# Kernel tuning notes

Hardware: AMD Instinct MI355X
Metric: run time of the kernel (lower is better)

Reference implementation:

```python
import jax, jax.numpy as jnp
import numpy as np

ALPHA, GAMMA = 0.25, 2.0            # focal loss params (cfg defaults)
W_CLASS, W_BBOX, W_GIOU = 2.0, 5.0, 2.0
N_CANDIDATE_K = 5                   # top-k ious used to derive dynamic k
CENTER_RADIUS = 2.5
B, Q, G, C = 32, 2000, 64, 80
IMG_W, IMG_H = 1333.0, 800.0


def _box_iou(a, b):
    # a: [Q,4] xyxy, b: [G,4] xyxy -> iou [Q,G], union [Q,G]
    area_a = (a[:, 2] - a[:, 0]) * (a[:, 3] - a[:, 1])
    area_b = (b[:, 2] - b[:, 0]) * (b[:, 3] - b[:, 1])
    lt = jnp.maximum(a[:, None, :2], b[None, :, :2])
    rb = jnp.minimum(a[:, None, 2:], b[None, :, 2:])
    wh = jnp.clip(rb - lt, 0.0)
    inter = wh[..., 0] * wh[..., 1]
    union = area_a[:, None] + area_b[None, :] - inter
    return inter / union, union


def _generalized_box_iou(a, b):
    iou, union = _box_iou(a, b)
    lt = jnp.minimum(a[:, None, :2], b[None, :, :2])
    rb = jnp.maximum(a[:, None, 2:], b[None, :, 2:])
    wh = jnp.clip(rb - lt, 0.0)
    area_c = wh[..., 0] * wh[..., 1]
    return iou - (area_c - union) / area_c


def _get_in_boxes_info(boxes, gt):
    # boxes, gt: absolute xyxy. Anchor centers inside gt box / inside center region.
    cx = (boxes[:, 0] + boxes[:, 2]) * 0.5
    cy = (boxes[:, 1] + boxes[:, 3]) * 0.5
    is_in_boxes = ((cx[:, None] > gt[None, :, 0]) & (cx[:, None] < gt[None, :, 2]) &
                   (cy[:, None] > gt[None, :, 1]) & (cy[:, None] < gt[None, :, 3]))
    gt_cx = (gt[:, 0] + gt[:, 2]) * 0.5
    gt_cy = (gt[:, 1] + gt[:, 3]) * 0.5
    gt_w = gt[:, 2] - gt[:, 0]
    gt_h = gt[:, 3] - gt[:, 1]
    is_in_centers = ((cx[:, None] > (gt_cx - CENTER_RADIUS * gt_w)[None, :]) &
                     (cx[:, None] < (gt_cx + CENTER_RADIUS * gt_w)[None, :]) &
                     (cy[:, None] > (gt_cy - CENTER_RADIUS * gt_h)[None, :]) &
                     (cy[:, None] < (gt_cy + CENTER_RADIUS * gt_h)[None, :]))
    fg_mask = is_in_boxes.any(1) | is_in_centers.any(1)
    return fg_mask, is_in_boxes & is_in_centers


def _dedup(cost, matching):
    # queries matched to >1 gt keep only their min-cost gt
    over = matching.sum(1) > 1
    keep = jax.nn.one_hot(jnp.argmin(cost, axis=1), cost.shape[1], dtype=matching.dtype)
    return jnp.where(over[:, None], keep, matching)


def _dynamic_k_matching(cost, ious):
    Qn, Gn = cost.shape
    topk_ious = jax.lax.top_k(ious.T, N_CANDIDATE_K)[0]              # [G,k]
    dynamic_ks = jnp.maximum(topk_ious.sum(1).astype(jnp.int32), 1)  # [G]
    # rank of each query within each gt's cost column (ascending)
    ranks = jnp.argsort(jnp.argsort(cost, axis=0), axis=0)
    matching = (ranks < dynamic_ks[None, :]).astype(cost.dtype)      # [Q,G]
    matching = _dedup(cost, matching)

    # ensure every gt gets >=1 query; bounded loop replaces data-dependent while
    def body(_, carry):
        cost_c, match_c = carry
        unmatched = match_c.sum(0) == 0                              # [G]
        any_un = unmatched.any()
        matched_q = match_c.sum(1) > 0
        cost_n = cost_c + jnp.where(matched_q, 1e5, 0.0)[:, None]
        add = jax.nn.one_hot(jnp.argmin(cost_n, axis=0), Qn, dtype=match_c.dtype).T
        match_n = jnp.maximum(match_c, add * unmatched[None, :].astype(match_c.dtype))
        match_n = _dedup(cost_n, match_n)
        return (jnp.where(any_un, cost_n, cost_c), jnp.where(any_un, match_n, match_c))

    cost, matching = jax.lax.fori_loop(0, Gn, body, (cost, matching))
    masked = jnp.where(matching > 0, cost, jnp.inf)
    matched_query_id = jnp.argmin(masked, axis=0)                    # [G]
    return matching, matched_query_id


def _match_one(logits, boxes, tgt_ids, gt_boxes, size_out, size_tgt):
    fg_mask, in_bc = _get_in_boxes_info(boxes, gt_boxes)
    ious, _ = _box_iou(boxes, gt_boxes)                              # [Q,G]
    neg = (1.0 - ALPHA) * logits ** GAMMA * (-jnp.log(1.0 - logits + 1e-8))
    pos = ALPHA * (1.0 - logits) ** GAMMA * (-jnp.log(logits + 1e-8))
    cost_class = jnp.take(pos - neg, tgt_ids, axis=1)                # [Q,G]
    out_n = boxes / size_out                                         # [Q,4]
    tgt_n = gt_boxes / size_tgt                                      # [G,4]
    cost_bbox = jnp.abs(out_n[:, None, :] - tgt_n[None, :, :]).sum(-1)  # L1 cdist
    cost_giou = -_generalized_box_iou(boxes, gt_boxes)
    cost = (W_BBOX * cost_bbox + W_CLASS * cost_class + W_GIOU * cost_giou
            + 100.0 * (~in_bc).astype(cost_bbox.dtype))
    cost = cost + jnp.where(fg_mask, 0.0, 1e4)[:, None]
    return _dynamic_k_matching(cost, ious)


def _rand_boxes(key, n_shape):
    k1, k2 = jax.random.split(key)
    wh = jnp.array([IMG_W, IMG_H], jnp.float32)
    ctr = jax.random.uniform(k1, n_shape + (2,)) * wh
    size = jax.random.uniform(k2, n_shape + (2,)) * (wh * 0.3) + 8.0
    x1y1 = jnp.clip(ctr - size * 0.5, 0.0, wh)
    x2y2 = jnp.clip(ctr + size * 0.5, 0.0, wh)
    x2y2 = jnp.maximum(x2y2, x1y1 + 1.0)
    return jnp.concatenate([x1y1, x2y2], axis=-1)


def setup_inputs() -> dict:
    key = jax.random.key(0)
    k1, k2, k3, k4 = jax.random.split(key, 4)
    pred_logits = jax.random.uniform(k1, (B, Q, C), minval=1e-4, maxval=1.0 - 1e-4)
    pred_boxes = _rand_boxes(k2, (B, Q))
    gt_classes = jax.random.randint(k3, (B, G), 0, C)
    gt_boxes = _rand_boxes(k4, (B, G))
    sz = jnp.array([IMG_W, IMG_H, IMG_W, IMG_H], jnp.float32)
    return {
        'pred_logits': pred_logits,
        'pred_boxes': pred_boxes,
        'gt_classes': gt_classes,
        'gt_boxes': gt_boxes,
        'image_size_xyxy': jnp.tile(sz, (B, 1)),
        'image_size_xyxy_tgt': jnp.tile(sz, (B, G, 1)),
    }


def reference(pred_logits, pred_boxes, gt_classes, gt_boxes, image_size_xyxy, image_size_xyxy_tgt):
    # matching: [B,Q,G] 0/1 assignment matrix (row q matched to gt g);
    # matched_query_id: [B,G] best query per gt. Padded-G, fixed-shape analog of
    # the per-image variable-length (indices, matched_ids) lists.
    matching, matched_query_id = jax.vmap(_match_one)(
        pred_logits, pred_boxes, gt_classes, gt_boxes, image_size_xyxy, image_size_xyxy_tgt)
    return matching, matched_query_id
```

## Files before the change

### kernel.cpp

```cpp
#include <hip/hip_runtime.h>
#include <cmath>

#pragma clang fp contract(off)

#define BB 32
#define QQ 2000
#define GG 64
#define CCH 80
#define TOPC 16
#define QT 32

typedef unsigned long long u64;

__global__ __launch_bounds__(256) void cost_kernel(
    const float* __restrict__ logits, const float* __restrict__ boxes,
    const int* __restrict__ gtc, const float* __restrict__ gtb,
    const float* __restrict__ szout, const float* __restrict__ sztgt,
    float* __restrict__ cost, int* __restrict__ rowarg,
    float* __restrict__ out_match) {
#pragma clang fp contract(off)
  const int b = blockIdx.y;
  const int q0 = blockIdx.x * QT;
  const int t = threadIdx.x;
  const int w = t >> 6, lane = t & 63;

  __shared__ float4 s_qb[QT];
  __shared__ float4 s_qn[QT];
  __shared__ float s_tile[QT * 65];

  const int gbase = (b * GG + lane) * 4;
  const float g0 = gtb[gbase + 0], g1 = gtb[gbase + 1];
  const float g2 = gtb[gbase + 2], g3 = gtb[gbase + 3];
  const float t0 = g0 / sztgt[gbase + 0], t1 = g1 / sztgt[gbase + 1];
  const float t2 = g2 / sztgt[gbase + 2], t3 = g3 / sztgt[gbase + 3];
  const float garea = (g2 - g0) * (g3 - g1);
  const float gcx = (g0 + g2) * 0.5f, gcy = (g1 + g3) * 0.5f;
  const float gw = g2 - g0, gh = g3 - g1;
  const float cxlo = gcx - 2.5f * gw, cxhi = gcx + 2.5f * gw;
  const float cylo = gcy - 2.5f * gh, cyhi = gcy + 2.5f * gh;
  const int cls = gtc[b * GG + lane];

  if (t < QT) {
    int q = q0 + t;
    float4 bx = (q < QQ) ? reinterpret_cast<const float4*>(boxes)[b * QQ + q]
                         : make_float4(0.f, 0.f, 1.f, 1.f);
    s_qb[t] = bx;
    float4 on;
    on.x = bx.x / szout[b * 4 + 0];
    on.y = bx.y / szout[b * 4 + 1];
    on.z = bx.z / szout[b * 4 + 2];
    on.w = bx.w / szout[b * 4 + 3];
    s_qn[t] = on;
  }

  const float* lbase = logits + (size_t)b * QQ * CCH;
  float pv[8];
  #pragma unroll
  for (int i = 0; i < 8; ++i) {
    int q = q0 + w * 8 + i;
    pv[i] = (q < QQ) ? lbase[(size_t)q * CCH + cls] : 0.5f;
  }
  __syncthreads();

  #pragma unroll
  for (int i = 0; i < 8; ++i) {
    const int qi = w * 8 + i;
    float4 bx = s_qb[qi];
    float4 on = s_qn[qi];
    float x1 = bx.x, y1 = bx.y, x2 = bx.z, y2 = bx.w;
    float cx = (x1 + x2) * 0.5f, cy = (y1 + y2) * 0.5f;
    float areaa = (x2 - x1) * (y2 - y1);

    bool ib = (cx > g0) & (cx < g2) & (cy > g1) & (cy < g3);
    bool ic = (cx > cxlo) & (cx < cxhi) & (cy > cylo) & (cy < cyhi);
    bool fg = (__ballot(ib) != 0ull) || (__ballot(ic) != 0ull);
    float fgadd = fg ? 0.0f : 1e4f;

    float ltx = fmaxf(x1, g0), lty = fmaxf(y1, g1);
    float rbx = fminf(x2, g2), rby = fminf(y2, g3);
    float iw = fmaxf(rbx - ltx, 0.0f), ih = fmaxf(rby - lty, 0.0f);
    float inter = iw * ih;
    float uni = (areaa + garea) - inter;
    float iou = inter / uni;
    float ex1 = fminf(x1, g0), ey1 = fminf(y1, g1);
    float ex2 = fmaxf(x2, g2), ey2 = fmaxf(y2, g3);
    float ew = fmaxf(ex2 - ex1, 0.0f), eh = fmaxf(ey2 - ey1, 0.0f);
    float areac = ew * eh;
    float giou = iou - (areac - uni) / areac;

    float p = pv[i];
    float negc = (0.75f * (p * p)) * (-logf((1.0f - p) + 1e-8f));
    float posc = (0.25f * ((1.0f - p) * (1.0f - p))) * (-logf(p + 1e-8f));
    float ccls = posc - negc;

    float cb = ((fabsf(on.x - t0) + fabsf(on.y - t1)) + fabsf(on.z - t2)) + fabsf(on.w - t3);
    float notbc = (ib & ic) ? 0.0f : 1.0f;
    float c = ((5.0f * cb + 2.0f * ccls) + 2.0f * (-giou)) + 100.0f * notbc;
    c = c + fgadd;

    s_tile[qi * 65 + lane] = c;
  }
  __syncthreads();

  if (t < QT) {
    int q = q0 + t;
    if (q < QQ) {
      const float* row = &s_tile[t * 65];
      float bv = row[0]; int bg = 0;
      #pragma unroll
      for (int g = 1; g < GG; ++g) {
        float cv = row[g];
        if (cv < bv) { bv = cv; bg = g; }
      }
      rowarg[b * QQ + q] = bg;
    }
  }

  float* cb_out = cost + (size_t)b * GG * QQ;
  const int qi = t & 31;
  const int q = q0 + qi;
  if (q < QQ) {
    #pragma unroll
    for (int pass = 0; pass < 8; ++pass) {
      int g = (t >> 5) + pass * 8;
      cb_out[(size_t)g * QQ + q] = s_tile[qi * 65 + g];
    }
  }

  int nq = QQ - q0; if (nq > QT) nq = QT;
  if (nq > 0) {
    float4* zb = reinterpret_cast<float4*>(out_match + ((size_t)b * QQ + q0) * GG);
    int n4 = nq * GG / 4;
    float4 z = make_float4(0.f, 0.f, 0.f, 0.f);
    for (int i = t; i < n4; i += 256) zb[i] = z;
  }
}

template <int TOPN>
__device__ __forceinline__ void block_select(
    u64 (&K)[8], int tid, u64* s_tmin, u64* s_cmin, u64* s_surv,
    u64* s_sorted, u64* s_thr, int* s_ns) {
  u64 m = K[0];
  #pragma unroll
  for (int j = 1; j < 8; ++j) m = (K[j] < m) ? K[j] : m;
  s_tmin[tid] = m;
  if (tid == 0) *s_ns = 0;
  __syncthreads();

  if (tid < 64) {
    u64 c = s_tmin[tid];
    u64 c1 = s_tmin[tid + 64], c2 = s_tmin[tid + 128], c3 = s_tmin[tid + 192];
    c = (c1 < c) ? c1 : c; c = (c2 < c) ? c2 : c; c = (c3 < c) ? c3 : c;
    s_cmin[tid] = c;
    int r = 0;
    for (int j = 0; j < 64; ++j) r += (s_cmin[j] < c) ? 1 : 0;
    if (r == TOPN - 1) *s_thr = c;
  }
  __syncthreads();

  const u64 t = *s_thr;
  int n = 0;
  #pragma unroll
  for (int j = 0; j < 8; ++j) n += (K[j] <= t) ? 1 : 0;
  if (n) {
    int base = atomicAdd(s_ns, n);
    int k = 0;
    #pragma unroll
    for (int j = 0; j < 8; ++j) if (K[j] <= t) s_surv[base + (k++)] = K[j];
  }
  __syncthreads();

  const int ns = *s_ns;
  if (ns <= 64) {
    if (tid < ns && tid < 64) {
      u64 k = s_surv[tid];
      int r = 0;
      for (int j = 0; j < ns; ++j) r += (s_surv[j] < k) ? 1 : 0;
      if (r < TOPN) s_sorted[r] = k;
    }
  } else if (tid < 64) {
    for (int pass = 0; pass < TOPN; ++pass) {
      u64 bk = ~0ull;
      for (int idx = tid; idx < ns; idx += 64) {
        u64 v = s_surv[idx]; bk = (v < bk) ? v : bk;
      }
      for (int off = 32; off; off >>= 1) {
        u64 ok = __shfl_down(bk, off, 64); bk = (ok < bk) ? ok : bk;
      }
      bk = __shfl(bk, 0, 64);
      for (int idx = tid; idx < ns; idx += 64)
        if (s_surv[idx] == bk) s_surv[idx] = ~0ull;
      if (tid == 0) s_sorted[pass] = bk;
    }
  }
  __syncthreads();
}

__global__ __launch_bounds__(256) void pick_kernel(
    const float* __restrict__ boxes, const float* __restrict__ gtb,
    const float* __restrict__ cost, short* __restrict__ lists,
    int* __restrict__ dynks) {
#pragma clang fp contract(off)
  const int bc = blockIdx.x;
  const int b = bc >> 6, col = bc & 63;
  const int tid = threadIdx.x;

  __shared__ u64 s_tmin[256];
  __shared__ u64 s_cmin[64];
  __shared__ u64 s_surv[512];
  __shared__ u64 s_sorted[TOPC];
  __shared__ u64 s_thr;
  __shared__ int s_ns;

  const int gbase = (b * GG + col) * 4;
  const float gx1 = gtb[gbase + 0], gy1 = gtb[gbase + 1];
  const float gx2 = gtb[gbase + 2], gy2 = gtb[gbase + 3];
  const float ga = (gx2 - gx1) * (gy2 - gy1);

  u64 K[8];
  #pragma unroll
  for (int j = 0; j < 8; ++j) {
    int q = tid * 8 + j;
    float val = -1e30f;
    if (q < QQ) {
      float4 bx = reinterpret_cast<const float4*>(boxes)[b * QQ + q];
      float areaa = (bx.z - bx.x) * (bx.w - bx.y);
      float ltx = fmaxf(bx.x, gx1), lty = fmaxf(bx.y, gy1);
      float rbx = fminf(bx.z, gx2), rby = fminf(bx.w, gy2);
      float iw = fmaxf(rbx - ltx, 0.0f), ih = fmaxf(rby - lty, 0.0f);
      float inter = iw * ih;
      val = inter / ((areaa + ga) - inter);
    }
    unsigned u = __float_as_uint(val);
    u = (u & 0x80000000u) ? ~u : (u | 0x80000000u);
    K[j] = ~(((u64)u << 16) | (u64)(0xFFFF - q));
  }
  block_select<5>(K, tid, s_tmin, s_cmin, s_surv, s_sorted, &s_thr, &s_ns);
  if (tid == 0) {
    float s = 0.0f;
    for (int r = 0; r < 5; ++r) {
      u64 kk = ~s_sorted[r];
      unsigned u = (unsigned)(kk >> 16);
      u = (u & 0x80000000u) ? (u & 0x7FFFFFFFu) : ~u;
      s += __uint_as_float(u);
    }
    int dynk = (int)s;
    if (dynk < 1) dynk = 1;
    dynks[bc] = dynk;
  }

  const float* ccol = cost + (size_t)bc * QQ;
  {
    float cv[8];
    if (tid < 249) {
      const float4* c4 = reinterpret_cast<const float4*>(ccol) + tid * 2;
      float4 a = c4[0], d = c4[1];
      cv[0] = a.x; cv[1] = a.y; cv[2] = a.z; cv[3] = a.w;
      cv[4] = d.x; cv[5] = d.y; cv[6] = d.z; cv[7] = d.w;
    } else {
      #pragma unroll
      for (int j = 0; j < 8; ++j) {
        int q = tid * 8 + j;
        cv[j] = (q < QQ) ? ccol[q] : INFINITY;
      }
    }
    #pragma unroll
    for (int j = 0; j < 8; ++j) {
      unsigned u = __float_as_uint(cv[j]);
      u = (u & 0x80000000u) ? ~u : (u | 0x80000000u);
      K[j] = ((u64)u << 16) | (u64)(tid * 8 + j);
    }
  }
  block_select<TOPC>(K, tid, s_tmin, s_cmin, s_surv, s_sorted, &s_thr, &s_ns);
  if (tid < TOPC) lists[bc * TOPC + tid] = (short)(s_sorted[tid] & 0xFFFFull);
}

__global__ __launch_bounds__(256) void serial_kernel(
    const float* __restrict__ cost, const short* __restrict__ lists,
    const int* __restrict__ dynks, const int* __restrict__ rowarg,
    float* __restrict__ out_match, float* __restrict__ out_ids) {
#pragma clang fp contract(off)
  const int b = blockIdx.x;
  const int tid = threadIdx.x;

  __shared__ unsigned s_mlo[QQ], s_mhi[QQ];
  __shared__ int s_first[QQ];
  __shared__ int s_pushed[QQ];
  __shared__ short s_rarg[QQ];
  __shared__ short s_list[GG * TOPC];
  __shared__ int s_cnt[GG];
  __shared__ short s_chosen[GG];
  __shared__ unsigned long long s_pack[GG];
  __shared__ int s_added[GG];
  __shared__ short s_ucols[GG];
  __shared__ short s_fb[GG];
  __shared__ int s_nadd, s_nfb, s_Tv;

  for (int q = tid; q < QQ; q += 256) {
    s_mlo[q] = 0u; s_mhi[q] = 0u; s_first[q] = -1; s_pushed[q] = -1;
    s_rarg[q] = (short)rowarg[b * QQ + q];
  }
  for (int i = tid; i < GG * TOPC; i += 256) s_list[i] = lists[b * GG * TOPC + i];
  if (tid < GG) s_cnt[tid] = 0;
  __syncthreads();

  if (tid < GG) {
    int dynk = dynks[b * GG + tid];
    s_cnt[tid] = dynk;
    for (int i = 0; i < dynk; ++i) {
      int q = s_list[tid * TOPC + i];
      if (tid < 32) atomicOr(&s_mlo[q], 1u << tid);
      else          atomicOr(&s_mhi[q], 1u << (tid - 32));
      s_first[q] = 0;
    }
  }
  __syncthreads();

  for (int q = tid; q < QQ; q += 256) {
    unsigned lo = s_mlo[q], hi = s_mhi[q];
    if (__popc(lo) + __popc(hi) > 1) {
      int bg = s_rarg[q];
      unsigned tl = lo, th = hi;
      while (tl) { int g = __ffs(tl) - 1; tl &= tl - 1; if (g != bg) atomicSub(&s_cnt[g], 1); }
      while (th) { int g = __ffs(th) + 31; th &= th - 1; if (g != bg) atomicSub(&s_cnt[g], 1); }
      bool had = (bg < 32) ? ((lo >> bg) & 1u) : ((hi >> (bg - 32)) & 1u);
      if (!had) atomicAdd(&s_cnt[bg], 1);
      s_mlo[q] = (bg < 32) ? (1u << bg) : 0u;
      s_mhi[q] = (bg >= 32) ? (1u << (bg - 32)) : 0u;
    }
  }
  __syncthreads();

  const float* costb = cost + (size_t)b * GG * QQ;

  if (tid < 64) {
    const int lane = tid;
    int T = 0;
    for (int iter = 0; iter < GG; ++iter) {
      unsigned long long bal = __ballot(s_cnt[lane] > 0);
      unsigned long long um = ~bal;
      if (um == 0ull) break;
      T++;

      bool isun = (um >> lane) & 1ull;
      int nu = __popcll(um);
      int pos = __popcll(um & ((1ull << lane) - 1ull));
      if (isun) s_ucols[pos] = (short)lane;
      if (lane == 0) { s_nfb = 0; s_nadd = 0; }

      const int sg = lane >> 4, li = lane & 15;
      for (int base = 0; base < nu; base += 4) {
        int ci = base + sg;
        int col = (ci < nu) ? (int)s_ucols[ci] : -1;
        bool cand_un = false; int cq = 0;
        if (col >= 0) {
          cq = s_list[col * TOPC + li];
          cand_un = ((s_mlo[cq] | s_mhi[cq]) == 0u);
        }
        unsigned long long bb = __ballot(cand_un);
        unsigned sub = (unsigned)((bb >> (sg * 16)) & 0xFFFFull);
        if (col >= 0) {
          if (sub) {
            if (li == __ffs(sub) - 1) s_chosen[col] = (short)cq;
          } else if (li == 0) {
            int slot = atomicAdd(&s_nfb, 1);
            s_fb[slot] = (short)col;
          }
        }
      }

      int nfb = s_nfb;
      for (int fi = 0; fi < nfb; ++fi) {
        int col = s_fb[fi];
        const float* ccol = costb + (size_t)col * QQ;
        float bv = INFINITY; int bq = 0x7fffffff;
        for (int q2 = lane; q2 < QQ; q2 += 64) {
          if ((s_mlo[q2] | s_mhi[q2]) == 0u) {
            float cv = ccol[q2];
            if (cv < bv) { bv = cv; bq = q2; }
          }
        }
        for (int off = 32; off; off >>= 1) {
          float ov = __shfl_down(bv, off, 64); int oq = __shfl_down(bq, off, 64);
          if (ov < bv || (ov == bv && oq < bq)) { bv = ov; bq = oq; }
        }
        bq = __shfl(bq, 0, 64);
        if (bq == 0x7fffffff) {
          bv = INFINITY; bq = 0x7fffffff;
          for (int q2 = lane; q2 < QQ; q2 += 64) {
            float cv = ccol[q2];
            int k = (s_first[q2] >= 0) ? (iter + 1 - s_first[q2]) : 0;
            for (int tt = 0; tt < k; ++tt) cv += 1e5f;
            if (cv < bv) { bv = cv; bq = q2; }
          }
          for (int off = 32; off; off >>= 1) {
            float ov = __shfl_down(bv, off, 64); int oq = __shfl_down(bq, off, 64);
            if (ov < bv || (ov == bv && oq < bq)) { bv = ov; bq = oq; }
          }
          bq = __shfl(bq, 0, 64);
        }
        if (lane == 0) s_chosen[col] = (short)bq;
      }

      if (isun) {
        int q = s_chosen[lane];
        if (lane < 32) atomicOr(&s_mlo[q], 1u << lane);
        else           atomicOr(&s_mhi[q], 1u << (lane - 32));
        atomicAdd(&s_cnt[lane], 1);
        if (s_first[q] == -1) s_first[q] = iter + 1;
        if (atomicExch(&s_pushed[q], iter) != iter) {
          int slot = atomicAdd(&s_nadd, 1);
          s_added[slot] = q;
        }
      }

      int na = s_nadd;
      if (lane < na) {
        int q = s_added[lane];
        unsigned lo = s_mlo[q], hi = s_mhi[q];
        if (__popc(lo) + __popc(hi) > 1) {
          int bg = s_rarg[q];
          unsigned tl = lo, th = hi;
          while (tl) { int g = __ffs(tl) - 1; tl &= tl - 1; if (g != bg) atomicSub(&s_cnt[g], 1); }
          while (th) { int g = __ffs(th) + 31; th &= th - 1; if (g != bg) atomicSub(&s_cnt[g], 1); }
          bool had = (bg < 32) ? ((lo >> bg) & 1u) : ((hi >> (bg - 32)) & 1u);
          if (!had) atomicAdd(&s_cnt[bg], 1);
          s_mlo[q] = (bg < 32) ? (1u << bg) : 0u;
          s_mhi[q] = (bg >= 32) ? (1u << (bg - 32)) : 0u;
        }
      }
    }
    if (tid == 0) s_Tv = T;
  }
  __syncthreads();
  const int T = s_Tv;

  if (tid < GG) s_pack[tid] = 0xFFFFFFFFFFFFFFFFull;
  __syncthreads();
  for (int q = tid; q < QQ; q += 256) {
    unsigned lo = s_mlo[q], hi = s_mhi[q];
    if (lo | hi) {
      int g = lo ? (__ffs(lo) - 1) : (__ffs(hi) + 31);
      float cv = costb[(size_t)g * QQ + q];
      int k = T - s_first[q];
      for (int tt = 0; tt < k; ++tt) cv += 1e5f;
      unsigned ub = __float_as_uint(cv);
      ub = (ub & 0x80000000u) ? ~ub : (ub | 0x80000000u);
      unsigned long long pk = ((unsigned long long)ub << 16) | (unsigned)q;
      atomicMin(&s_pack[g], pk);
    }
  }
  __syncthreads();
  if (tid < GG) {
    unsigned long long pk = s_pack[tid];
    out_ids[b * GG + tid] =
        (pk == 0xFFFFFFFFFFFFFFFFull) ? 0.0f : (float)(pk & 0xFFFFull);
  }
  for (int q = tid; q < QQ; q += 256) {
    unsigned lo = s_mlo[q], hi = s_mhi[q];
    if (lo | hi) {
      int g = lo ? (__ffs(lo) - 1) : (__ffs(hi) + 31);
      out_match[((size_t)b * QQ + q) * GG + g] = 1.0f;
    }
  }
}

extern "C" void kernel_launch(void* const* d_in, const int* in_sizes, int n_in,
                              void* d_out, int out_size, void* d_ws, size_t ws_size,
                              hipStream_t stream) {
  const float* logits = (const float*)d_in[0];
  const float* boxes  = (const float*)d_in[1];
  const int*   gtc    = (const int*)d_in[2];
  const float* gtbx   = (const float*)d_in[3];
  const float* szout  = (const float*)d_in[4];
  const float* sztgt  = (const float*)d_in[5];
  float* out = (float*)d_out;

  const size_t matchN  = (size_t)BB * QQ * GG;
  const size_t rowargN = (size_t)BB * QQ;
  const size_t listsN  = (size_t)BB * GG * TOPC;

  char* p = (char*)d_ws;
  float* cost   = (float*)p;          p += matchN * 4;
  int*   rowarg = (int*)p;            p += rowargN * 4;
  short* lists  = (short*)p;          p += listsN * 2;
  int*   dynks  = (int*)p;

  float* out_ids = out + matchN;

  hipLaunchKernelGGL(cost_kernel, dim3((QQ + QT - 1) / QT, BB), dim3(256), 0, stream,
                     logits, boxes, gtc, gtbx, szout, sztgt, cost, rowarg, out);
  hipLaunchKernelGGL(pick_kernel, dim3(BB * GG), dim3(256), 0, stream,
                     boxes, gtbx, cost, lists, dynks);
  hipLaunchKernelGGL(serial_kernel, dim3(BB), dim3(256), 0, stream,
                     cost, lists, dynks, rowarg, out, out_ids);
}
```

Before: 127.6 us.

## Restructure serial matching loop with per-lane candidate registers and matched-byte mask

The single-wave iterative matching loop now keeps each gt column's 16 top candidates in registers and tests them against a byte-per-query 'matched' mask. This replaces the cooperative 4-columns-per-pass ballot scan and the shared compaction arrays. Fallback columns are picked directly from a ballot bitmask, and the chosen query stays in a register. Duplicate detection drops the per-query atomicExch push array and uses a linear scan over the added list. The aim is to cut shared-memory traffic and synchronisation inside the latency-bound serial loop. The trade-off is extra per-lane work in the quadratic duplicate scan and the new mask, which is never cleared when a query is deduplicated.

```diff
diff --git a/kernel.cpp b/kernel.cpp
--- a/kernel.cpp
+++ b/kernel.cpp
@@ -285,33 +285,30 @@
 
   __shared__ unsigned s_mlo[QQ], s_mhi[QQ];
   __shared__ int s_first[QQ];
-  __shared__ int s_pushed[QQ];
+  __shared__ unsigned char s_mq[QQ];
   __shared__ short s_rarg[QQ];
-  __shared__ short s_list[GG * TOPC];
   __shared__ int s_cnt[GG];
-  __shared__ short s_chosen[GG];
-  __shared__ unsigned long long s_pack[GG];
+  __shared__ u64 s_pack[GG];
   __shared__ int s_added[GG];
-  __shared__ short s_ucols[GG];
-  __shared__ short s_fb[GG];
-  __shared__ int s_nadd, s_nfb, s_Tv;
+  __shared__ int s_nadd, s_Tv;
 
   for (int q = tid; q < QQ; q += 256) {
-    s_mlo[q] = 0u; s_mhi[q] = 0u; s_first[q] = -1; s_pushed[q] = -1;
+    s_mlo[q] = 0u; s_mhi[q] = 0u; s_first[q] = -1; s_mq[q] = 0;
     s_rarg[q] = (short)rowarg[b * QQ + q];
   }
-  for (int i = tid; i < GG * TOPC; i += 256) s_list[i] = lists[b * GG * TOPC + i];
   if (tid < GG) s_cnt[tid] = 0;
   __syncthreads();
 
   if (tid < GG) {
     int dynk = dynks[b * GG + tid];
     s_cnt[tid] = dynk;
+    const short* lrow = lists + (b * GG + tid) * TOPC;
     for (int i = 0; i < dynk; ++i) {
-      int q = s_list[tid * TOPC + i];
+      int q = lrow[i];
       if (tid < 32) atomicOr(&s_mlo[q], 1u << tid);
       else          atomicOr(&s_mhi[q], 1u << (tid - 32));
       s_first[q] = 0;
+      s_mq[q] = 1;
     }
   }
   __syncthreads();
@@ -335,47 +332,43 @@
 
   if (tid < 64) {
     const int lane = tid;
+    unsigned cand[8];
+    {
+      const unsigned* lrow =
+          reinterpret_cast<const unsigned*>(lists + (b * GG + lane) * TOPC);
+      #pragma unroll
+      for (int j = 0; j < 8; ++j) cand[j] = lrow[j];
+    }
     int T = 0;
     for (int iter = 0; iter < GG; ++iter) {
       unsigned long long bal = __ballot(s_cnt[lane] > 0);
       unsigned long long um = ~bal;
       if (um == 0ull) break;
       T++;
-
       bool isun = (um >> lane) & 1ull;
-      int nu = __popcll(um);
-      int pos = __popcll(um & ((1ull << lane) - 1ull));
-      if (isun) s_ucols[pos] = (short)lane;
-      if (lane == 0) { s_nfb = 0; s_nadd = 0; }
-
-      const int sg = lane >> 4, li = lane & 15;
-      for (int base = 0; base < nu; base += 4) {
-        int ci = base + sg;
-        int col = (ci < nu) ? (int)s_ucols[ci] : -1;
-        bool cand_un = false; int cq = 0;
-        if (col >= 0) {
-          cq = s_list[col * TOPC + li];
-          cand_un = ((s_mlo[cq] | s_mhi[cq]) == 0u);
-        }
-        unsigned long long bb = __ballot(cand_un);
-        unsigned sub = (unsigned)((bb >> (sg * 16)) & 0xFFFFull);
-        if (col >= 0) {
-          if (sub) {
-            if (li == __ffs(sub) - 1) s_chosen[col] = (short)cq;
-          } else if (li == 0) {
-            int slot = atomicAdd(&s_nfb, 1);
-            s_fb[slot] = (short)col;
-          }
-        }
-      }
-
-      int nfb = s_nfb;
-      for (int fi = 0; fi < nfb; ++fi) {
-        int col = s_fb[fi];
+      if (lane == 0) s_nadd = 0;
+
+      int myq = -1;
+      unsigned fmask = 0;
+      if (isun) {
+        #pragma unroll
+        for (int i = 0; i < 16; ++i) {
+          int cq = (cand[i >> 1] >> (16 * (i & 1))) & 0xFFFF;
+          fmask |= ((unsigned)(s_mq[cq] == 0)) << i;
+        }
+        if (fmask) {
+          int idx = __ffs(fmask) - 1;
+          myq = (cand[idx >> 1] >> (16 * (idx & 1))) & 0xFFFF;
+        }
+      }
+
+      unsigned long long fb = __ballot(isun && fmask == 0);
+      while (fb) {
+        int col = __ffsll(fb) - 1; fb &= fb - 1;
         const float* ccol = costb + (size_t)col * QQ;
         float bv = INFINITY; int bq = 0x7fffffff;
         for (int q2 = lane; q2 < QQ; q2 += 64) {
-          if ((s_mlo[q2] | s_mhi[q2]) == 0u) {
+          if (s_mq[q2] == 0) {
             float cv = ccol[q2];
             if (cv < bv) { bv = cv; bq = q2; }
           }
@@ -399,34 +392,37 @@
           }
           bq = __shfl(bq, 0, 64);
         }
-        if (lane == 0) s_chosen[col] = (short)bq;
+        if (lane == col) myq = bq;
       }
 
       if (isun) {
-        int q = s_chosen[lane];
+        int q = myq;
         if (lane < 32) atomicOr(&s_mlo[q], 1u << lane);
         else           atomicOr(&s_mhi[q], 1u << (lane - 32));
         atomicAdd(&s_cnt[lane], 1);
-        if (s_first[q] == -1) s_first[q] = iter + 1;
-        if (atomicExch(&s_pushed[q], iter) != iter) {
-          int slot = atomicAdd(&s_nadd, 1);
-          s_added[slot] = q;
-        }
+        if (s_first[q] < 0) s_first[q] = iter + 1;
+        s_mq[q] = 1;
+        int slot = atomicAdd(&s_nadd, 1);
+        s_added[slot] = q;
       }
 
       int na = s_nadd;
       if (lane < na) {
         int q = s_added[lane];
-        unsigned lo = s_mlo[q], hi = s_mhi[q];
-        if (__popc(lo) + __popc(hi) > 1) {
-          int bg = s_rarg[q];
-          unsigned tl = lo, th = hi;
-          while (tl) { int g = __ffs(tl) - 1; tl &= tl - 1; if (g != bg) atomicSub(&s_cnt[g], 1); }
-          while (th) { int g = __ffs(th) + 31; th &= th - 1; if (g != bg) atomicSub(&s_cnt[g], 1); }
-          bool had = (bg < 32) ? ((lo >> bg) & 1u) : ((hi >> (bg - 32)) & 1u);
-          if (!had) atomicAdd(&s_cnt[bg], 1);
-          s_mlo[q] = (bg < 32) ? (1u << bg) : 0u;
-          s_mhi[q] = (bg >= 32) ? (1u << (bg - 32)) : 0u;
+        bool dup = false;
+        for (int j = 0; j < lane; ++j) dup = dup || (s_added[j] == q);
+        if (!dup) {
+          unsigned lo = s_mlo[q], hi = s_mhi[q];
+          if (__popc(lo) + __popc(hi) > 1) {
+            int bg = s_rarg[q];
+            unsigned tl = lo, th = hi;
+            while (tl) { int g = __ffs(tl) - 1; tl &= tl - 1; if (g != bg) atomicSub(&s_cnt[g], 1); }
+            while (th) { int g = __ffs(th) + 31; th &= th - 1; if (g != bg) atomicSub(&s_cnt[g], 1); }
+            bool had = (bg < 32) ? ((lo >> bg) & 1u) : ((hi >> (bg - 32)) & 1u);
+            if (!had) atomicAdd(&s_cnt[bg], 1);
+            s_mlo[q] = (bg < 32) ? (1u << bg) : 0u;
+            s_mhi[q] = (bg >= 32) ? (1u << (bg - 32)) : 0u;
+          }
         }
       }
     }
@@ -446,13 +442,13 @@
       for (int tt = 0; tt < k; ++tt) cv += 1e5f;
       unsigned ub = __float_as_uint(cv);
       ub = (ub & 0x80000000u) ? ~ub : (ub | 0x80000000u);
-      unsigned long long pk = ((unsigned long long)ub << 16) | (unsigned)q;
+      u64 pk = ((u64)ub << 16) | (unsigned)q;
       atomicMin(&s_pack[g], pk);
     }
   }
   __syncthreads();
   if (tid < GG) {
-    unsigned long long pk = s_pack[tid];
+    u64 pk = s_pack[tid];
     out_ids[b * GG + tid] =
         (pk == 0xFFFFFFFFFFFFFFFFull) ? 0.0f : (float)(pk & 0xFFFFull);
   }
```

After: 127.0 us, median of 2. No clear change (-0.4%).
